# Kernel optimization log

Hardware: AMD Instinct MI355X
Metric: run time of the kernel (lower is better)

Reference implementation:

```python
import jax, jax.numpy as jnp
import numpy as np

B, S, IN = 4, 4096, 2048
E, D, A, R = 16, 128, 128, 4  # num_experts, expert_vector_dim, attn_dim, mlp_rank
LN_EPS = 1e-5


def _ln2(x, g, b):
    # LayerNorm over the last two dims [E, D] jointly (torch nn.LayerNorm([E, D]))
    mu = x.mean(axis=(-2, -1), keepdims=True)
    var = ((x - mu) ** 2).mean(axis=(-2, -1), keepdims=True)
    return (x - mu) * jax.lax.rsqrt(var + LN_EPS) * g + b


def setup_inputs() -> dict:
    key = jax.random.key(0)
    ks = jax.random.split(key, 8)
    f32 = jnp.float32
    return {
        "hidden_states": jax.random.normal(ks[0], (B, S, IN), f32),
        "expert_embedding": jax.random.normal(ks[1], (E, D), f32) * 0.02,
        "ln_gamma": jnp.ones((E, D), f32),
        "ln_beta": jnp.zeros((E, D), f32),
        "Wv_w": jax.random.normal(ks[2], (E, IN), f32) * 0.02,
        "Wv_b": jnp.zeros((E,), f32),
        "mlp_w1": jax.random.normal(ks[3], (R, IN), f32) * 0.02,
        "mlp_b1": jnp.zeros((R,), f32),
        "mlp_w2": jax.random.normal(ks[4], (E * D, R), f32) * 0.02,
        "mlp_b2": jnp.zeros((E * D,), f32),
        "te_Wq": jax.random.normal(ks[5], (A, D), f32) * 0.05,
        "te_Wk": jax.random.normal(ks[6], (A, D), f32) * 0.05,
        "top_k": 2,
    }


def reference(hidden_states, expert_embedding, ln_gamma, ln_beta, Wv_w, Wv_b,
              mlp_w1, mlp_b1, mlp_w2, mlp_b2, te_Wq, te_Wk, top_k):
    # global expert vectors, layernormed over [E, D]: (E, D)
    ge = _ln2(expert_embedding[None, None], ln_gamma, ln_beta)[0, 0]
    # input gate = W_v(hidden): (B, S, E)
    input_gate = jnp.einsum('bsi,ei->bse', hidden_states, Wv_w) + Wv_b
    # TE mlp -> dynamic per-token expert vectors: (B, S, E, D)
    h = jax.nn.relu(jnp.einsum('bsi,ri->bsr', hidden_states, mlp_w1) + mlp_b1)
    dyn = (jnp.einsum('bsr,or->bso', h, mlp_w2) + mlp_b2).reshape(B, S, E, D)
    dyn = _ln2(dyn, ln_gamma, ln_beta)
    # attention-style routing: Q from dyn experts, K from global experts
    q = jnp.einsum('bsed,ad->bsea', dyn, te_Wq)     # (B, S, E, A)
    k = jnp.einsum('ed,ad->ea', ge, te_Wk)          # (E, A)
    scale = 1.0 / float(np.sqrt(A))
    sim = jax.nn.softmax(jnp.einsum('bsqa,ka->bsqk', q, k) * scale, axis=-1)
    gate = jnp.einsum('bsqk,bsk->bsq', sim, input_gate)
    rw = jax.nn.softmax(gate, axis=-1)              # (B, S, E)
    # top-k masking + sharpened softmax (temperature 0.1)
    vals, idx = jax.lax.top_k(rw, top_k)            # (B, S, k)
    oh = jax.nn.one_hot(idx, E, dtype=rw.dtype)     # (B, S, k, E)
    scattered = jnp.einsum('bske,bsk->bse', oh, vals)
    keep = oh.sum(axis=-2) > 0
    neg = jnp.finfo(rw.dtype).min
    masked = jnp.where(keep, scattered, neg)
    return jax.nn.softmax(masked / 0.1, axis=-1)
```

## Files before the change

### kernel.cpp

```cpp
#include <hip/hip_runtime.h>
#include <math.h>

#define NTOK   16384
#define INDIM  2048
#define NROWS  20
#define CHUNK  256

#define WS_PKT  0
#define WS_D1K  1024
#define WS_GQK  1280
#define WS_BQK  1536
#define WS_SCAL 1792
#define WS_TOT  1818

#define SIM_SCALE 0.08838834764831845f

#define LBUF1   5120
#define LRED2_STRIDE 324
#define LRED    5440

__device__ __forceinline__ void async16(const float* g, float* l) {
    __builtin_amdgcn_global_load_lds(
        (const __attribute__((address_space(1))) void*)g,
        (__attribute__((address_space(3))) void*)l, 16, 0, 0);
}

__device__ __forceinline__ void stage_w(const float* __restrict__ wv,
                                        const float* __restrict__ w1,
                                        float* ldsw, int wave, int lane, int goff) {
    const int l4 = lane << 2;
    #pragma unroll
    for (int j = 0; j < 5; ++j) {
        const int r = wave + (j << 2);
        const float* src = (j < 4) ? (wv + (r << 11)) : (w1 + ((r - 16) << 11));
        async16(src + goff + l4, ldsw + r * CHUNK + l4);
    }
}

__device__ __forceinline__ void load_h(float4 h[4], const float* __restrict__ hb,
                                       int goff) {
    #pragma unroll
    for (int t = 0; t < 4; ++t)
        h[t] = *(const float4*)(hb + t * INDIM + goff);
}

__device__ __forceinline__ void compute_chunk(float acc[NROWS][4],
                                              const float* wb,
                                              const float4 h[4]) {
    #pragma unroll
    for (int w = 0; w < NROWS; ++w) {
        float4 wf = *(const float4*)(wb + (w << 8));
        #pragma unroll
        for (int t = 0; t < 4; ++t) {
            acc[w][t] = fmaf(h[t].x, wf.x,
                        fmaf(h[t].y, wf.y,
                        fmaf(h[t].z, wf.z,
                        fmaf(h[t].w, wf.w, acc[w][t]))));
        }
    }
}

__global__ __launch_bounds__(256) void hr_pre2(
    const float* __restrict__ ee, const float* __restrict__ gam,
    const float* __restrict__ bta, const float* __restrict__ w2,
    const float* __restrict__ b2, const float* __restrict__ wq,
    const float* __restrict__ wk, float* __restrict__ ws)
{
    const int tid  = threadIdx.x;
    const int bx   = blockIdx.x;
    const int lane = tid & 63;
    const int wave = tid >> 6;

    if (bx == 16) {
        __shared__ float sacc[26];
        if (tid < 26) sacc[tid] = 0.f;
        __syncthreads();
        float pa[26];
        #pragma unroll
        for (int j = 0; j < 26; ++j) pa[j] = 0.f;
        for (int i = tid; i < 2048; i += 256) {
            float b = b2[i];
            float4 w4 = *(const float4*)(w2 + i * 4);
            float wr[4] = {w4.x, w4.y, w4.z, w4.w};
            pa[0] += b;
            pa[1] += b * b;
            #pragma unroll
            for (int r = 0; r < 4; ++r) {
                pa[2 + r] += wr[r];
                pa[6 + r] += b * wr[r];
                #pragma unroll
                for (int r2 = 0; r2 < 4; ++r2) pa[10 + r * 4 + r2] += wr[r] * wr[r2];
            }
        }
        #pragma unroll
        for (int j = 0; j < 26; ++j) {
            float v = pa[j];
            v += __shfl_xor(v, 32); v += __shfl_xor(v, 16); v += __shfl_xor(v, 8);
            v += __shfl_xor(v, 4);  v += __shfl_xor(v, 2);  v += __shfl_xor(v, 1);
            if (lane == 0) atomicAdd(&sacc[j], v);
        }
        __syncthreads();
        if (tid < 26) ws[WS_SCAL + tid] = sacc[tid] * (1.f / 2048.f);
        return;
    }

    const int e2 = bx;
    __shared__ float sge[128];
    __shared__ float sK[128];
    __shared__ float sWqK[128];
    __shared__ float sred[8];

    float v8[8];
    float s = 0.f;
    #pragma unroll
    for (int j = 0; j < 8; ++j) { v8[j] = ee[tid + j * 256]; s += v8[j]; }
    s += __shfl_xor(s, 32); s += __shfl_xor(s, 16); s += __shfl_xor(s, 8);
    s += __shfl_xor(s, 4);  s += __shfl_xor(s, 2);  s += __shfl_xor(s, 1);
    if (lane == 0) sred[wave] = s;
    __syncthreads();
    const float mu = (sred[0] + sred[1] + sred[2] + sred[3]) * (1.f / 2048.f);
    float q = 0.f;
    #pragma unroll
    for (int j = 0; j < 8; ++j) { float d = v8[j] - mu; q += d * d; }
    q += __shfl_xor(q, 32); q += __shfl_xor(q, 16); q += __shfl_xor(q, 8);
    q += __shfl_xor(q, 4);  q += __shfl_xor(q, 2);  q += __shfl_xor(q, 1);
    if (lane == 0) sred[4 + wave] = q;
    __syncthreads();
    const float rsq = rsqrtf((sred[4] + sred[5] + sred[6] + sred[7]) * (1.f / 2048.f) + 1e-5f);

    if (tid < 128) {
        int idx = (e2 << 7) + tid;
        sge[tid] = (ee[idx] - mu) * rsq * gam[idx] + bta[idx];
    }
    __syncthreads();

    {
        int a = tid >> 1, half = tid & 1;
        const float* wr = wk + (a << 7) + (half << 6);
        const float* gg = sge + (half << 6);
        float acc = 0.f;
        #pragma unroll 8
        for (int j = 0; j < 64; ++j) acc = fmaf(gg[j], wr[j], acc);
        acc += __shfl_xor(acc, 1);
        if (half == 0) sK[a] = acc;
    }
    __syncthreads();

    {
        int d = tid >> 1, half = tid & 1;
        float acc = 0.f;
        #pragma unroll 8
        for (int j = 0; j < 64; ++j) {
            int a = (half << 6) + j;
            acc = fmaf(wq[(a << 7) + d], sK[a], acc);
        }
        acc += __shfl_xor(acc, 1);
        if (half == 0) sWqK[d] = acc;
    }
    __syncthreads();

    {
        int o = tid >> 2, qd = tid & 3;
        int r = o >> 4, e = o & 15;
        float acc = 0.f;
        #pragma unroll 8
        for (int j = 0; j < 32; ++j) {
            int d  = (qd << 5) + j;
            int ed = (e << 7) + d;
            acc = fmaf(w2[ed * 4 + r] * gam[ed], sWqK[d], acc);
        }
        acc += __shfl_xor(acc, 1);
        acc += __shfl_xor(acc, 2);
        if (qd == 0) ws[WS_PKT + (e2 << 6) + (r << 4) + e] = acc;
    }

    if (tid < 192) {
        int kind = tid >> 6;
        int e    = (tid >> 2) & 15;
        int qd   = tid & 3;
        float acc = 0.f;
        #pragma unroll 8
        for (int j = 0; j < 32; ++j) {
            int d  = (qd << 5) + j;
            int ed = (e << 7) + d;
            float w = sWqK[d];
            float t = (kind == 0) ? b2[ed] * gam[ed]
                    : (kind == 1) ? gam[ed]
                                  : bta[ed];
            acc = fmaf(t, w, acc);
        }
        acc += __shfl_xor(acc, 1);
        acc += __shfl_xor(acc, 2);
        if (qd == 0) ws[WS_D1K + (kind << 8) + (e2 << 4) + e] = acc;
    }
}

__global__ __launch_bounds__(256) void hr_main(
    const float* __restrict__ hidden, const float* __restrict__ wv,
    const float* __restrict__ wvb, const float* __restrict__ w1,
    const float* __restrict__ b1, const float* __restrict__ tab,
    float* __restrict__ out)
{
    __shared__ float lds[10240];

    const int tid  = threadIdx.x;
    const int wave = tid >> 6;
    const int lane = tid & 63;
    const int tok0 = (blockIdx.x << 4) + (wave << 2);
    const float* hb = hidden + (size_t)tok0 * INDIM + (lane << 2);

    float acc[NROWS][4];
    #pragma unroll
    for (int w = 0; w < NROWS; ++w) {
        acc[w][0] = 0.f; acc[w][1] = 0.f; acc[w][2] = 0.f; acc[w][3] = 0.f;
    }

    const float* wr0 = &lds[lane << 2];
    const float* wr1 = &lds[LBUF1 + (lane << 2)];

    float4 hc[4], hn[4];
    stage_w(wv, w1, lds, wave, lane, 0);
    load_h(hc, hb, 0);
    __syncthreads();

    for (int cc = 0; cc < 4; ++cc) {
        const int c1 = 2 * cc + 1;
        stage_w(wv, w1, lds + LBUF1, wave, lane, c1 << 8);
        load_h(hn, hb, c1 << 8);
        compute_chunk(acc, wr0, hc);
        __syncthreads();
        if (cc != 3) {
            stage_w(wv, w1, lds, wave, lane, (c1 + 1) << 8);
            load_h(hc, hb, (c1 + 1) << 8);
        }
        compute_chunk(acc, wr1, hn);
        __syncthreads();
    }

    #pragma unroll
    for (int w = 0; w < NROWS; ++w) {
        #pragma unroll
        for (int t = 0; t < 4; ++t) {
            float v = acc[w][t];
            v += __shfl_xor(v, 32);
            v += __shfl_xor(v, 16);
            acc[w][t] = v;
        }
    }
    {
        const int q = lane >> 4, i = lane & 15;
        #pragma unroll
        for (int w = 0; w < NROWS; ++w) {
            if (q == w / 5) {
                #pragma unroll
                for (int t = 0; t < 4; ++t)
                    lds[((wave << 2) + t) * LRED2_STRIDE + (w << 4) + i] = acc[w][t];
            }
        }
    }
    __syncthreads();

    #pragma unroll
    for (int pp = 0; pp < 2; ++pp) {
        const int p = tid + pp * 256;
        if (p < 320) {
            const int w = p >> 4, tok = p & 15;
            const float4* rp = (const float4*)&lds[tok * LRED2_STRIDE + (w << 4)];
            float4 r0 = rp[0], r1 = rp[1], r2 = rp[2], r3 = rp[3];
            float s = (r0.x + r0.y + r0.z + r0.w) + (r1.x + r1.y + r1.z + r1.w)
                    + (r2.x + r2.y + r2.z + r2.w) + (r3.x + r3.y + r3.z + r3.w);
            lds[LRED + tok * 20 + w] = s;
        }
    }
    __syncthreads();

    const int tok = tid >> 4;
    const int e   = tid & 15;

    float ig[16];
    #pragma unroll
    for (int j = 0; j < 16; ++j) ig[j] = lds[LRED + tok * 20 + j] + wvb[j];
    float h[4];
    #pragma unroll
    for (int r = 0; r < 4; ++r) h[r] = fmaxf(lds[LRED + tok * 20 + 16 + r] + b1[r], 0.f);

    float muT = tab[WS_SCAL + 0];
    float e2m = tab[WS_SCAL + 1];
    #pragma unroll
    for (int r = 0; r < 4; ++r) {
        muT = fmaf(h[r], tab[WS_SCAL + 2 + r], muT);
        e2m = fmaf(2.f * h[r], tab[WS_SCAL + 6 + r], e2m);
        #pragma unroll
        for (int r2 = 0; r2 < 4; ++r2)
            e2m = fmaf(h[r] * h[r2], tab[WS_SCAL + 10 + r * 4 + r2], e2m);
    }
    const float var = e2m - muT * muT;
    const float rsq = rsqrtf(var + 1e-5f);

    float sv[16];
    #pragma unroll
    for (int e2 = 0; e2 < 16; ++e2) {
        float s = tab[WS_D1K + (e2 << 4) + e];
        s = fmaf(h[0], tab[(e2 << 6) + e], s);
        s = fmaf(h[1], tab[(e2 << 6) + 16 + e], s);
        s = fmaf(h[2], tab[(e2 << 6) + 32 + e], s);
        s = fmaf(h[3], tab[(e2 << 6) + 48 + e], s);
        s = fmaf(-muT, tab[WS_GQK + (e2 << 4) + e], s);
        sv[e2] = (rsq * s + tab[WS_BQK + (e2 << 4) + e]) * SIM_SCALE;
    }
    float mx = sv[0];
    #pragma unroll
    for (int e2 = 1; e2 < 16; ++e2) mx = fmaxf(mx, sv[e2]);
    float den = 0.f, gate = 0.f;
    #pragma unroll
    for (int e2 = 0; e2 < 16; ++e2) {
        float p = __expf(sv[e2] - mx);
        den += p;
        gate = fmaf(p, ig[e2], gate);
    }
    gate /= den;

    float gm = gate;
    gm = fmaxf(gm, __shfl_xor(gm, 1));
    gm = fmaxf(gm, __shfl_xor(gm, 2));
    gm = fmaxf(gm, __shfl_xor(gm, 4));
    gm = fmaxf(gm, __shfl_xor(gm, 8));
    float ex = __expf(gate - gm);
    float es = ex;
    es += __shfl_xor(es, 1);
    es += __shfl_xor(es, 2);
    es += __shfl_xor(es, 4);
    es += __shfl_xor(es, 8);
    const float rw = ex / es;

    float v1 = rw; int i1 = e;
    #pragma unroll
    for (int m = 1; m <= 8; m <<= 1) {
        float ov = __shfl_xor(v1, m);
        int   oi = __shfl_xor(i1, m);
        if (ov > v1 || (ov == v1 && oi < i1)) { v1 = ov; i1 = oi; }
    }
    float v2 = (e == i1) ? -INFINITY : rw; int i2 = e;
    #pragma unroll
    for (int m = 1; m <= 8; m <<= 1) {
        float ov = __shfl_xor(v2, m);
        int   oi = __shfl_xor(i2, m);
        if (ov > v2 || (ov == v2 && oi < i2)) { v2 = ov; i2 = oi; }
    }

    float oval = 0.f;
    if (e == i1 || e == i2) {
        float t = __expf((v2 - v1) * 10.f);
        oval = (e == i1) ? (1.f / (1.f + t)) : (t / (1.f + t));
    }
    out[(((size_t)blockIdx.x << 4) + tok) * 16 + e] = oval;
}

extern "C" void kernel_launch(void* const* d_in, const int* in_sizes, int n_in,
                              void* d_out, int out_size, void* d_ws, size_t ws_size,
                              hipStream_t stream)
{
    const float* hidden = (const float*)d_in[0];
    const float* ee     = (const float*)d_in[1];
    const float* gam    = (const float*)d_in[2];
    const float* bta    = (const float*)d_in[3];
    const float* wv     = (const float*)d_in[4];
    const float* wvb    = (const float*)d_in[5];
    const float* w1     = (const float*)d_in[6];
    const float* b1     = (const float*)d_in[7];
    const float* w2     = (const float*)d_in[8];
    const float* b2     = (const float*)d_in[9];
    const float* wq     = (const float*)d_in[10];
    const float* wk     = (const float*)d_in[11];
    float* out = (float*)d_out;
    float* ws  = (float*)d_ws;

    hipLaunchKernelGGL(hr_pre2, dim3(17), dim3(256), 0, stream,
                       ee, gam, bta, w2, b2, wq, wk, ws);
    hipLaunchKernelGGL(hr_main, dim3(NTOK / 16), dim3(256), 0, stream,
                       hidden, wv, wvb, w1, b1, ws, out);
}
```

Measured before the change: 240.8 us.

## Load projection weights directly into registers instead of double-buffered LDS staging

Drops the async global-to-LDS double-buffered staging of the 20 weight rows and the per-chunk block barriers. Each thread now loads its float4 slice of the weights straight from global (L2/L1-cached) into registers each chunk, while prefetching the next hidden chunk. LDS shrinks, which may allow more blocks per CU, but every wave now issues its own weight loads and uses more VGPRs for the 20 float4 weights, with less latency hiding.

```diff
diff --git a/kernel.cpp b/kernel.cpp
--- a/kernel.cpp
+++ b/kernel.cpp
@@ -15,26 +15,11 @@
 
 #define SIM_SCALE 0.08838834764831845f
 
-#define LBUF1   5120
 #define LRED2_STRIDE 324
 #define LRED    5440
 
-__device__ __forceinline__ void async16(const float* g, float* l) {
-    __builtin_amdgcn_global_load_lds(
-        (const __attribute__((address_space(1))) void*)g,
-        (__attribute__((address_space(3))) void*)l, 16, 0, 0);
-}
-
-__device__ __forceinline__ void stage_w(const float* __restrict__ wv,
-                                        const float* __restrict__ w1,
-                                        float* ldsw, int wave, int lane, int goff) {
-    const int l4 = lane << 2;
-    #pragma unroll
-    for (int j = 0; j < 5; ++j) {
-        const int r = wave + (j << 2);
-        const float* src = (j < 4) ? (wv + (r << 11)) : (w1 + ((r - 16) << 11));
-        async16(src + goff + l4, ldsw + r * CHUNK + l4);
-    }
+__device__ __forceinline__ float fma4(float4 a, float4 b, float acc) {
+    return fmaf(a.x, b.x, fmaf(a.y, b.y, fmaf(a.z, b.z, fmaf(a.w, b.w, acc))));
 }
 
 __device__ __forceinline__ void load_h(float4 h[4], const float* __restrict__ hb,
@@ -42,22 +27,6 @@
     #pragma unroll
     for (int t = 0; t < 4; ++t)
         h[t] = *(const float4*)(hb + t * INDIM + goff);
-}
-
-__device__ __forceinline__ void compute_chunk(float acc[NROWS][4],
-                                              const float* wb,
-                                              const float4 h[4]) {
-    #pragma unroll
-    for (int w = 0; w < NROWS; ++w) {
-        float4 wf = *(const float4*)(wb + (w << 8));
-        #pragma unroll
-        for (int t = 0; t < 4; ++t) {
-            acc[w][t] = fmaf(h[t].x, wf.x,
-                        fmaf(h[t].y, wf.y,
-                        fmaf(h[t].z, wf.z,
-                        fmaf(h[t].w, wf.w, acc[w][t]))));
-        }
-    }
 }
 
 __global__ __launch_bounds__(256) void hr_pre2(
@@ -201,13 +170,16 @@
     const float* __restrict__ b1, const float* __restrict__ tab,
     float* __restrict__ out)
 {
-    __shared__ float lds[10240];
+    __shared__ float lds[5760];
 
     const int tid  = threadIdx.x;
     const int wave = tid >> 6;
     const int lane = tid & 63;
     const int tok0 = (blockIdx.x << 4) + (wave << 2);
-    const float* hb = hidden + (size_t)tok0 * INDIM + (lane << 2);
+    const int l4   = lane << 2;
+    const float* hb  = hidden + (size_t)tok0 * INDIM + l4;
+    const float* wvl = wv + l4;
+    const float* w1l = w1 + l4;
 
     float acc[NROWS][4];
     #pragma unroll
@@ -215,26 +187,30 @@
         acc[w][0] = 0.f; acc[w][1] = 0.f; acc[w][2] = 0.f; acc[w][3] = 0.f;
     }
 
-    const float* wr0 = &lds[lane << 2];
-    const float* wr1 = &lds[LBUF1 + (lane << 2)];
-
-    float4 hc[4], hn[4];
-    stage_w(wv, w1, lds, wave, lane, 0);
-    load_h(hc, hb, 0);
-    __syncthreads();
-
-    for (int cc = 0; cc < 4; ++cc) {
-        const int c1 = 2 * cc + 1;
-        stage_w(wv, w1, lds + LBUF1, wave, lane, c1 << 8);
-        load_h(hn, hb, c1 << 8);
-        compute_chunk(acc, wr0, hc);
-        __syncthreads();
-        if (cc != 3) {
-            stage_w(wv, w1, lds, wave, lane, (c1 + 1) << 8);
-            load_h(hc, hb, (c1 + 1) << 8);
-        }
-        compute_chunk(acc, wr1, hn);
-        __syncthreads();
+    float4 h[4], hn[4];
+    load_h(h, hb, 0);
+
+    #pragma unroll 1
+    for (int c = 0; c < 8; ++c) {
+        const int goff = c << 8;
+        float4 w[NROWS];
+        #pragma unroll
+        for (int r = 0; r < 16; ++r)
+            w[r] = *(const float4*)(wvl + (r << 11) + goff);
+        #pragma unroll
+        for (int r = 0; r < 4; ++r)
+            w[16 + r] = *(const float4*)(w1l + (r << 11) + goff);
+        if (c < 7) load_h(hn, hb, goff + CHUNK);
+        #pragma unroll
+        for (int r = 0; r < NROWS; ++r) {
+            #pragma unroll
+            for (int t = 0; t < 4; ++t)
+                acc[r][t] = fma4(h[t], w[r], acc[r][t]);
+        }
+        if (c < 7) {
+            #pragma unroll
+            for (int t = 0; t < 4; ++t) h[t] = hn[t];
+        }
     }
 
     #pragma unroll
@@ -280,19 +256,19 @@
     float ig[16];
     #pragma unroll
     for (int j = 0; j < 16; ++j) ig[j] = lds[LRED + tok * 20 + j] + wvb[j];
-    float h[4];
-    #pragma unroll
-    for (int r = 0; r < 4; ++r) h[r] = fmaxf(lds[LRED + tok * 20 + 16 + r] + b1[r], 0.f);
+    float h2[4];
+    #pragma unroll
+    for (int r = 0; r < 4; ++r) h2[r] = fmaxf(lds[LRED + tok * 20 + 16 + r] + b1[r], 0.f);
 
     float muT = tab[WS_SCAL + 0];
     float e2m = tab[WS_SCAL + 1];
     #pragma unroll
     for (int r = 0; r < 4; ++r) {
-        muT = fmaf(h[r], tab[WS_SCAL + 2 + r], muT);
-        e2m = fmaf(2.f * h[r], tab[WS_SCAL + 6 + r], e2m);
+        muT = fmaf(h2[r], tab[WS_SCAL + 2 + r], muT);
+        e2m = fmaf(2.f * h2[r], tab[WS_SCAL + 6 + r], e2m);
         #pragma unroll
         for (int r2 = 0; r2 < 4; ++r2)
-            e2m = fmaf(h[r] * h[r2], tab[WS_SCAL + 10 + r * 4 + r2], e2m);
+            e2m = fmaf(h2[r] * h2[r2], tab[WS_SCAL + 10 + r * 4 + r2], e2m);
     }
     const float var = e2m - muT * muT;
     const float rsq = rsqrtf(var + 1e-5f);
@@ -301,10 +277,10 @@
     #pragma unroll
     for (int e2 = 0; e2 < 16; ++e2) {
         float s = tab[WS_D1K + (e2 << 4) + e];
-        s = fmaf(h[0], tab[(e2 << 6) + e], s);
-        s = fmaf(h[1], tab[(e2 << 6) + 16 + e], s);
-        s = fmaf(h[2], tab[(e2 << 6) + 32 + e], s);
-        s = fmaf(h[3], tab[(e2 << 6) + 48 + e], s);
+        s = fmaf(h2[0], tab[(e2 << 6) + e], s);
+        s = fmaf(h2[1], tab[(e2 << 6) + 16 + e], s);
+        s = fmaf(h2[2], tab[(e2 << 6) + 32 + e], s);
+        s = fmaf(h2[3], tab[(e2 << 6) + 48 + e], s);
         s = fmaf(-muT, tab[WS_GQK + (e2 << 4) + e], s);
         sv[e2] = (rsq * s + tab[WS_BQK + (e2 << 4) + e]) * SIM_SCALE;
     }
```

Result: slower. 250.2 us (+3.9%).
